# Optimization experiments

Measured on AMD Instinct MI355X. Metric: run time of the kernel, lower is better.

## Reference

```python
import jax, jax.numpy as jnp
import numpy as np

B, D, N, K, V = 32, 256, 2048, 512, 6
COMMIT = 1.0

def setup_inputs() -> dict:
    key = jax.random.key(0)
    k1, k2 = jax.random.split(key)
    inputs = jax.random.normal(k1, (B, D, N), dtype=jnp.float32)
    embeddings = jax.random.normal(k2, (V, D, K), dtype=jnp.float32)
    return {"inputs": inputs, "embeddings": embeddings}

def _vq_layer(residual, emb):
    # residual: (B, D, N); emb: (D, K) codebook
    flat = residual.transpose(0, 2, 1).reshape(-1, D)                # (B*N, D)
    dist = (jnp.sum(flat * flat, axis=1, keepdims=True)
            + jnp.sum(emb * emb, axis=0, keepdims=True)
            - 2.0 * (flat @ emb))                                    # (B*N, K)
    idx = jnp.argmin(dist, axis=1)                                   # (B*N,)
    q = jnp.take(emb.T, idx, axis=0)                                 # (B*N, D) gather
    q = q.reshape(B, N, D).transpose(0, 2, 1)                        # (B, D, N)
    # straight-through estimator
    q_st = residual + jax.lax.stop_gradient(q - residual)
    loss = COMMIT * jnp.mean(jnp.square(jax.lax.stop_gradient(q) - residual))
    return q_st, idx.reshape(B, N), loss

def reference(inputs, embeddings):
    residual = inputs
    q_sum = jnp.zeros_like(inputs)
    tokens = []
    total_loss = jnp.float32(0.0)
    for v in range(V):  # fixed small layer stack
        q, idx, loss = _vq_layer(residual, embeddings[v])
        q_sum = q_sum + q
        tokens.append(idx)
        total_loss = total_loss + loss
        residual = residual - q
    return q_sum, jnp.stack(tokens, axis=0), total_loss
```

## Files before the change

### kernel.cpp

```cpp
#include <hip/hip_runtime.h>

#define B_  32
#define D_  256
#define N_  2048
#define K_  512
#define V_  6
#define DN_ (D_*N_)
#define DK_ (D_*K_)
#define QSZ (B_*D_*N_)
#define TOKSZ (B_*N_)
#define TOK_OFF QSZ
#define LOSS_OFF (QSZ + V_*TOKSZ)
#define MARGIN 0.02f
#define FCAP 16384
#define NBLK (TOKSZ/64)

typedef __attribute__((ext_vector_type(8))) short short8b;
typedef __attribute__((ext_vector_type(4))) float f32x4;

__device__ __forceinline__ unsigned short f2bf(float x) {
  unsigned u = __float_as_uint(x);
  unsigned r = (u + 0x7fffu + ((u >> 16) & 1u)) >> 16;
  return (unsigned short)r;
}
__device__ __forceinline__ float bf2f(unsigned short h) {
  return __uint_as_float(((unsigned)h) << 16);
}
__device__ __forceinline__ unsigned orderf(float f) {
  unsigned u = __float_as_uint(f);
  return (u >> 31) ? ~u : (u | 0x80000000u);
}
__device__ __forceinline__ float unorderf(unsigned u) {
  return __uint_as_float((u & 0x80000000u) ? (u & 0x7fffffffu) : ~u);
}
__device__ __forceinline__ unsigned long long shfl_xor_u64(unsigned long long v, int m) {
  int lo = __shfl_xor((int)(unsigned)(v & 0xffffffffull), m, 64);
  int hi = __shfl_xor((int)(unsigned)(v >> 32), m, 64);
  return ((unsigned long long)(unsigned)hi << 32) | (unsigned)lo;
}

__global__ __launch_bounds__(256) void pack_kernel(const float* __restrict__ emb,
                                                   float* __restrict__ Ef32,
                                                   unsigned short* __restrict__ Ehi,
                                                   unsigned short* __restrict__ Elo) {
  __shared__ float T[64][68];
  const int tid = threadIdx.x;
  const int k0 = blockIdx.x * 64, d0 = blockIdx.y * 64, v = blockIdx.z;
  const float* src = emb + (size_t)v * DK_;
  const int r = tid >> 4, c4 = (tid & 15) * 4;
  #pragma unroll
  for (int i = 0; i < 4; ++i) {
    int d = d0 + r + i * 16;
    float4 x = *(const float4*)(src + (size_t)d * K_ + k0 + c4);
    *(float4*)&T[r + i * 16][c4] = x;
  }
  __syncthreads();
  #pragma unroll
  for (int i = 0; i < 4; ++i) {
    int k = k0 + r + i * 16;
    float4 wv;
    wv.x = T[c4 + 0][r + i * 16];
    wv.y = T[c4 + 1][r + i * 16];
    wv.z = T[c4 + 2][r + i * 16];
    wv.w = T[c4 + 3][r + i * 16];
    size_t o = ((size_t)v * K_ + k) * 256 + d0 + c4;
    *(float4*)(Ef32 + o) = wv;
    ushort4 hv, lv;
    hv.x = f2bf(wv.x); lv.x = f2bf(wv.x - bf2f(hv.x));
    hv.y = f2bf(wv.y); lv.y = f2bf(wv.y - bf2f(hv.y));
    hv.z = f2bf(wv.z); lv.z = f2bf(wv.z - bf2f(hv.z));
    hv.w = f2bf(wv.w); lv.w = f2bf(wv.w - bf2f(hv.w));
    *(ushort4*)(Ehi + o) = hv;
    *(ushort4*)(Elo + o) = lv;
  }
}

__global__ __launch_bounds__(256) void en2_kernel(const float* __restrict__ Ef32,
                                                  float* __restrict__ en2f,
                                                  double* __restrict__ en2d) {
  __shared__ double P[64][4];
  const int tid = threadIdx.x;
  const int k = blockIdx.x * 64 + (tid >> 2), q = tid & 3;
  const float* e = Ef32 + (size_t)k * 256 + q * 64;
  double s = 0.0;
  #pragma unroll 8
  for (int i = 0; i < 64; ++i) { double x = (double)e[i]; s = fma(x, x, s); }
  P[tid >> 2][q] = s;
  __syncthreads();
  if (tid < 64) {
    int k2 = blockIdx.x * 64 + tid;
    double t = (P[tid][0] + P[tid][1]) + (P[tid][2] + P[tid][3]);
    en2d[k2] = t;
    en2f[k2] = (float)t;
  }
}

__global__ __launch_bounds__(256) void transpose_in(const float* __restrict__ in,
                                                    float* __restrict__ Rt) {
  __shared__ float T[64][68];
  const int tid = threadIdx.x;
  const int n0 = blockIdx.x * 64, d0 = blockIdx.y * 64, b = blockIdx.z;
  const float* src = in + (size_t)b * DN_;
  const int r = tid >> 4, c4 = (tid & 15) * 4;
  #pragma unroll
  for (int i = 0; i < 4; ++i) {
    int d = d0 + r + i * 16;
    float4 v = *(const float4*)(src + (size_t)d * N_ + n0 + c4);
    *(float4*)&T[r + i * 16][c4] = v;
  }
  __syncthreads();
  #pragma unroll
  for (int i = 0; i < 4; ++i) {
    int n = n0 + r + i * 16;
    float4 w;
    w.x = T[c4 + 0][r + i * 16];
    w.y = T[c4 + 1][r + i * 16];
    w.z = T[c4 + 2][r + i * 16];
    w.w = T[c4 + 3][r + i * 16];
    *(float4*)(Rt + ((size_t)b * N_ + n) * 256 + d0 + c4) = w;
  }
}

template <bool LAST>
__global__ __launch_bounds__(256, 2) void vq_mfma(
    float* __restrict__ Rt,
    const unsigned short* __restrict__ Ehi, const unsigned short* __restrict__ Elo,
    const float* __restrict__ Ef32v, const float* __restrict__ en2f,
    float* __restrict__ tokOut, float* __restrict__ lossPart,
    int* __restrict__ flagCnt, int* __restrict__ flagList)
{
  __shared__ unsigned short Ahi[8 * 2048];
  __shared__ unsigned short Alo[8 * 2048];
  __shared__ unsigned long long wmin[4][64];
  __shared__ float wsec[4][64];
  __shared__ int sIdx[64];
  __shared__ float wred[4];

  const int tid = threadIdx.x;
  const int lane = tid & 63, w = tid >> 6;
  const int l15 = lane & 15, lg = lane >> 4;
  const int gt0 = blockIdx.x * 64;
  float* rtBase = Rt + (size_t)gt0 * 256;
  const int kb = w * 128;

  const unsigned short* ehiL = Ehi + (size_t)(kb + l15) * 256 + lg * 8;
  const unsigned short* eloL = Elo + (size_t)(kb + l15) * 256 + lg * 8;

  const int stok = tid >> 2, sg = tid & 3;
  #pragma unroll
  for (int c = 0; c < 8; ++c) {
    float4 v0 = *(const float4*)(rtBase + (size_t)stok * 256 + c * 32 + sg * 8);
    float4 v1 = *(const float4*)(rtBase + (size_t)stok * 256 + c * 32 + sg * 8 + 4);
    float xs[8] = {v0.x, v0.y, v0.z, v0.w, v1.x, v1.y, v1.z, v1.w};
    short8b hv, lv;
    #pragma unroll
    for (int j = 0; j < 8; ++j) {
      unsigned short h = f2bf(xs[j]);
      hv[j] = (short)h;
      lv[j] = (short)f2bf(xs[j] - bf2f(h));
    }
    *(short8b*)&Ahi[c * 2048 + sg * 512 + stok * 8] = hv;
    *(short8b*)&Alo[c * 2048 + sg * 512 + stok * 8] = lv;
  }
  __syncthreads();

  f32x4 acc[4][8];
  #pragma unroll
  for (int tt = 0; tt < 4; ++tt)
    #pragma unroll
    for (int kt = 0; kt < 8; ++kt) acc[tt][kt] = (f32x4){0.f, 0.f, 0.f, 0.f};

  float en8[8];
  #pragma unroll
  for (int kt = 0; kt < 8; ++kt) en8[kt] = en2f[kb + kt * 16 + l15];

  #pragma unroll
  for (int c = 0; c < 8; ++c) {
    short8b ah[4], al[4];
    #pragma unroll
    for (int tt = 0; tt < 4; ++tt) {
      ah[tt] = *(const short8b*)&Ahi[c * 2048 + lg * 512 + (tt * 16 + l15) * 8];
      al[tt] = *(const short8b*)&Alo[c * 2048 + lg * 512 + (tt * 16 + l15) * 8];
    }
    #pragma unroll
    for (int kt = 0; kt < 8; ++kt) {
      short8b bh = *(const short8b*)(ehiL + (size_t)kt * 4096 + c * 32);
      short8b bl = *(const short8b*)(eloL + (size_t)kt * 4096 + c * 32);
      #pragma unroll
      for (int tt = 0; tt < 4; ++tt) {
        acc[tt][kt] = __builtin_amdgcn_mfma_f32_16x16x32_bf16(ah[tt], bh, acc[tt][kt], 0, 0, 0);
        acc[tt][kt] = __builtin_amdgcn_mfma_f32_16x16x32_bf16(ah[tt], bl, acc[tt][kt], 0, 0, 0);
        acc[tt][kt] = __builtin_amdgcn_mfma_f32_16x16x32_bf16(al[tt], bh, acc[tt][kt], 0, 0, 0);
      }
    }
  }

  #pragma unroll
  for (int tt = 0; tt < 4; ++tt)
    #pragma unroll
    for (int r = 0; r < 4; ++r) {
      const int token = tt * 16 + lg * 4 + r;
      float dv0 = en8[0] - 2.f * acc[tt][0][r];
      unsigned long long p = ((unsigned long long)orderf(dv0) << 32) | (unsigned)(kb + l15);
      float s = 3.402823466e+38f;
      #pragma unroll
      for (int kt = 1; kt < 8; ++kt) {
        float dv = en8[kt] - 2.f * acc[tt][kt][r];
        unsigned long long pk = ((unsigned long long)orderf(dv) << 32) |
                                (unsigned)(kb + kt * 16 + l15);
        if (pk < p) { s = fminf(s, unorderf((unsigned)(p >> 32))); p = pk; }
        else s = fminf(s, dv);
      }
      #pragma unroll
      for (int m = 1; m <= 8; m <<= 1) {
        unsigned long long po = shfl_xor_u64(p, m);
        float so = __shfl_xor(s, m, 64);
        unsigned long long pmax = (po < p) ? p : po;
        s = fminf(fminf(s, so), unorderf((unsigned)(pmax >> 32)));
        p = (po < p) ? po : p;
      }
      if (l15 == 0) { wmin[w][token] = p; wsec[w][token] = s; }
    }
  __syncthreads();
  if (tid < 64) {
    unsigned long long p = wmin[0][tid]; float s = wsec[0][tid];
    #pragma unroll
    for (int w2 = 1; w2 < 4; ++w2) {
      unsigned long long po = wmin[w2][tid]; float so = wsec[w2][tid];
      unsigned long long pmax = (po < p) ? p : po;
      s = fminf(fminf(s, so), unorderf((unsigned)(pmax >> 32)));
      p = (po < p) ? po : p;
    }
    int kwin = (int)(p & 0xffffffffull);
    sIdx[tid] = kwin;
    tokOut[gt0 + tid] = (float)kwin;
    float bd = unorderf((unsigned)(p >> 32));
    if (s - bd < MARGIN) {
      int pos = atomicAdd(flagCnt, 1);
      if (pos < FCAP) flagList[pos] = gt0 + tid;
    }
  }
  __syncthreads();

  const int uj = tid >> 2, q = tid & 3;
  const int kw = sIdx[uj];
  const float* er = Ef32v + (size_t)kw * 256 + q * 64;
  float* rr = rtBase + (size_t)uj * 256 + q * 64;
  float lacc = 0.f;
  #pragma unroll
  for (int i = 0; i < 8; ++i) {
    const int c = q * 2 + (i >> 2), g = i & 3;
    short8b h8 = *(const short8b*)&Ahi[c * 2048 + g * 512 + uj * 8];
    short8b l8 = *(const short8b*)&Alo[c * 2048 + g * 512 + uj * 8];
    float4 e0 = *(const float4*)(er + i * 8);
    float4 e1 = *(const float4*)(er + i * 8 + 4);
    float rn[8];
    rn[0] = bf2f((unsigned short)h8[0]) + bf2f((unsigned short)l8[0]) - e0.x;
    rn[1] = bf2f((unsigned short)h8[1]) + bf2f((unsigned short)l8[1]) - e0.y;
    rn[2] = bf2f((unsigned short)h8[2]) + bf2f((unsigned short)l8[2]) - e0.z;
    rn[3] = bf2f((unsigned short)h8[3]) + bf2f((unsigned short)l8[3]) - e0.w;
    rn[4] = bf2f((unsigned short)h8[4]) + bf2f((unsigned short)l8[4]) - e1.x;
    rn[5] = bf2f((unsigned short)h8[5]) + bf2f((unsigned short)l8[5]) - e1.y;
    rn[6] = bf2f((unsigned short)h8[6]) + bf2f((unsigned short)l8[6]) - e1.z;
    rn[7] = bf2f((unsigned short)h8[7]) + bf2f((unsigned short)l8[7]) - e1.w;
    if (!LAST) {
      *(float4*)(rr + i * 8)     = make_float4(rn[0], rn[1], rn[2], rn[3]);
      *(float4*)(rr + i * 8 + 4) = make_float4(rn[4], rn[5], rn[6], rn[7]);
    }
    #pragma unroll
    for (int j = 0; j < 8; ++j) lacc += rn[j] * rn[j];
  }
  #pragma unroll
  for (int m = 32; m >= 1; m >>= 1) lacc += __shfl_xor(lacc, m, 64);
  if (lane == 0) wred[w] = lacc;
  __syncthreads();
  if (tid == 0) lossPart[blockIdx.x] = (wred[0] + wred[1]) + (wred[2] + wred[3]);
}

__global__ __launch_bounds__(256) void fixup_kernel(
    const float* __restrict__ inputs, const float* __restrict__ Ef32,
    const double* __restrict__ en2d, float* __restrict__ Rt,
    float* __restrict__ tokens, const int* __restrict__ flagList,
    const int* __restrict__ flagCnt, int v)
{
  __shared__ double rD[256];
  __shared__ double sbd[256];
  __shared__ int sbk[256];
  __shared__ int snk;
  const int tid = threadIdx.x;
  int cnt = flagCnt[0]; if (cnt > FCAP) cnt = FCAP;
  const float* Ev = Ef32 + (size_t)v * DK_;
  for (int i = blockIdx.x; i < cnt; i += gridDim.x) {
    const int gt = flagList[i];
    const int b = gt >> 11, n = gt & (N_ - 1);
    double r = (double)inputs[(size_t)b * DN_ + (size_t)tid * N_ + n];
    for (int u = 0; u < v; ++u) {
      int tu = (int)tokens[u * TOKSZ + gt];
      r -= (double)Ef32[(size_t)u * DK_ + (size_t)tu * 256 + tid];
    }
    rD[tid] = r;
    __syncthreads();
    double best = 1.0e300; int bk = 0;
    #pragma unroll
    for (int half = 0; half < 2; ++half) {
      const int k = tid + half * 256;
      const float* e0 = Ev + (size_t)k * 256;
      double s0 = 0.0, s1 = 0.0, s2 = 0.0, s3 = 0.0;
      #pragma unroll 8
      for (int dd = 0; dd < 256; dd += 4) {
        s0 = fma(rD[dd + 0], (double)e0[dd + 0], s0);
        s1 = fma(rD[dd + 1], (double)e0[dd + 1], s1);
        s2 = fma(rD[dd + 2], (double)e0[dd + 2], s2);
        s3 = fma(rD[dd + 3], (double)e0[dd + 3], s3);
      }
      double dist = en2d[v * K_ + k] - 2.0 * ((s0 + s1) + (s2 + s3));
      if (dist < best) { best = dist; bk = k; }
    }
    sbd[tid] = best; sbk[tid] = bk;
    __syncthreads();
    for (int st = 128; st >= 1; st >>= 1) {
      if (tid < st) {
        double od = sbd[tid + st]; int ok = sbk[tid + st];
        if (od < sbd[tid] || (od == sbd[tid] && ok < sbk[tid])) {
          sbd[tid] = od; sbk[tid] = ok;
        }
      }
      __syncthreads();
    }
    if (tid == 0) {
      int nk = sbk[0];
      int old = (int)tokens[v * TOKSZ + gt];
      if (nk != old) { tokens[v * TOKSZ + gt] = (float)nk; snk = nk; }
      else snk = -1;
    }
    __syncthreads();
    if (snk >= 0)
      Rt[(size_t)gt * 256 + tid] = (float)(rD[tid] - (double)Ev[(size_t)snk * 256 + tid]);
    __syncthreads();
  }
}

__global__ __launch_bounds__(256) void finalize_q(const float* __restrict__ toks,
                                                  const float* __restrict__ Ef32,
                                                  float* __restrict__ out) {
  const int tid = threadIdx.x;
  const int gt = blockIdx.x * 64 + (tid >> 2);
  const int q = tid & 3;
  const int b = gt >> 11, n = gt & (N_ - 1);
  float4 a[16];
  int k0 = (int)toks[gt];
  const float* e0 = Ef32 + (size_t)k0 * 256 + q * 64;
  #pragma unroll
  for (int i = 0; i < 16; ++i) a[i] = ((const float4*)e0)[i];
  #pragma unroll
  for (int v = 1; v < V_; ++v) {
    int kv = (int)toks[v * TOKSZ + gt];
    const float* ev = Ef32 + (size_t)v * DK_ + (size_t)kv * 256 + q * 64;
    #pragma unroll
    for (int i = 0; i < 16; ++i) {
      float4 e = ((const float4*)ev)[i];
      a[i].x += e.x; a[i].y += e.y; a[i].z += e.z; a[i].w += e.w;
    }
  }
  float* dst = out + (size_t)b * DN_ + n;
  #pragma unroll
  for (int i = 0; i < 16; ++i) {
    int d = q * 64 + i * 4;
    dst[(size_t)(d + 0) * N_] = a[i].x;
    dst[(size_t)(d + 1) * N_] = a[i].y;
    dst[(size_t)(d + 2) * N_] = a[i].z;
    dst[(size_t)(d + 3) * N_] = a[i].w;
  }
}

__global__ __launch_bounds__(256) void loss_kernel(const float* __restrict__ part,
                                                   float* __restrict__ out) {
  __shared__ float s[256];
  const int tid = threadIdx.x;
  float a = 0.f;
  for (int i = tid; i < V_ * NBLK; i += 256) a += part[i];
  s[tid] = a;
  __syncthreads();
  for (int st = 128; st >= 1; st >>= 1) {
    if (tid < st) s[tid] += s[tid + st];
    __syncthreads();
  }
  if (tid == 0) out[LOSS_OFF] = s[0] * (1.0f / (float)QSZ);
}

extern "C" void kernel_launch(void* const* d_in, const int* in_sizes, int n_in,
                              void* d_out, int out_size, void* d_ws, size_t ws_size,
                              hipStream_t stream) {
  (void)in_sizes; (void)n_in; (void)out_size; (void)ws_size;
  const float* inputs = (const float*)d_in[0];
  const float* emb    = (const float*)d_in[1];
  float* out = (float*)d_out;
  char* ws = (char*)d_ws;

  unsigned short* Ehi = (unsigned short*)(ws + 0);
  unsigned short* Elo = (unsigned short*)(ws + 1572864);
  float*  Ef32 = (float*)(ws + 3145728);
  float*  en2f = (float*)(ws + 6291456);
  double* en2d = (double*)(ws + 6303744);
  float*  part = (float*)(ws + 6328320);
  int*    flagCnt  = (int*)(ws + 6352896);
  int*    flagList = (int*)(ws + 6352920);

  float* Rt   = out;
  float* toks = out + TOK_OFF;

  hipMemsetAsync(flagCnt, 0, V_ * sizeof(int), stream);
  pack_kernel<<<dim3(8, 4, 6), 256, 0, stream>>>(emb, Ef32, Ehi, Elo);
  en2_kernel<<<48, 256, 0, stream>>>(Ef32, en2f, en2d);
  transpose_in<<<dim3(32, 4, 32), 256, 0, stream>>>(inputs, Rt);

  for (int v = 0; v < V_; ++v) {
    const unsigned short* ehi = Ehi + (size_t)v * DK_;
    const unsigned short* elo = Elo + (size_t)v * DK_;
    const float* ef = Ef32 + (size_t)v * DK_;
    if (v < V_ - 1)
      vq_mfma<false><<<NBLK, 256, 0, stream>>>(Rt, ehi, elo, ef, en2f + v * K_,
                                               toks + v * TOKSZ, part + v * NBLK,
                                               flagCnt + v, flagList + v * FCAP);
    else
      vq_mfma<true><<<NBLK, 256, 0, stream>>>(Rt, ehi, elo, ef, en2f + v * K_,
                                              toks + v * TOKSZ, part + v * NBLK,
                                              flagCnt + v, flagList + v * FCAP);
    fixup_kernel<<<512, 256, 0, stream>>>(inputs, Ef32, en2d, Rt, toks,
                                          flagList + v * FCAP, flagCnt + v, v);
  }
  finalize_q<<<NBLK, 256, 0, stream>>>(toks, Ef32, out);
  loss_kernel<<<1, 256, 0, stream>>>(part, out);
}
```

Baseline: 879.6 us.

## Store residual as split bf16 hi/lo in global memory and halve tokens per block

The residual is now kept in global memory as pre-split bf16 hi/lo arrays instead of fp32. The MFMA kernel reads A fragments directly from global memory, so the per-block LDS staging and the conversion pass go away. Tokens per block drop from 64 to 32 and the occupancy hint rises to 4 blocks per CU, which gives more blocks and fewer accumulators per thread but less reuse of the codebook B loads per block. The residual update re-splits into hi/lo on write, and the fixup kernel writes the same format. The partial-loss buffer grows, so the flag offsets in the workspace move.

```diff
diff --git a/kernel.cpp b/kernel.cpp
--- a/kernel.cpp
+++ b/kernel.cpp
@@ -13,7 +13,8 @@
 #define LOSS_OFF (QSZ + V_*TOKSZ)
 #define MARGIN 0.02f
 #define FCAP 16384
-#define NBLK (TOKSZ/64)
+#define TPB_ 32
+#define NBLK (TOKSZ/TPB_)
 
 typedef __attribute__((ext_vector_type(8))) short short8b;
 typedef __attribute__((ext_vector_type(4))) float f32x4;
@@ -95,8 +96,9 @@
   }
 }
 
-__global__ __launch_bounds__(256) void transpose_in(const float* __restrict__ in,
-                                                    float* __restrict__ Rt) {
+__global__ __launch_bounds__(256) void split_in(const float* __restrict__ in,
+                                                unsigned short* __restrict__ Rhi,
+                                                unsigned short* __restrict__ Rlo) {
   __shared__ float T[64][68];
   const int tid = threadIdx.x;
   const int n0 = blockIdx.x * 64, d0 = blockIdx.y * 64, b = blockIdx.z;
@@ -117,86 +119,72 @@
     w.y = T[c4 + 1][r + i * 16];
     w.z = T[c4 + 2][r + i * 16];
     w.w = T[c4 + 3][r + i * 16];
-    *(float4*)(Rt + ((size_t)b * N_ + n) * 256 + d0 + c4) = w;
+    ushort4 hv, lv;
+    hv.x = f2bf(w.x); lv.x = f2bf(w.x - bf2f(hv.x));
+    hv.y = f2bf(w.y); lv.y = f2bf(w.y - bf2f(hv.y));
+    hv.z = f2bf(w.z); lv.z = f2bf(w.z - bf2f(hv.z));
+    hv.w = f2bf(w.w); lv.w = f2bf(w.w - bf2f(hv.w));
+    size_t o = ((size_t)b * N_ + n) * 256 + d0 + c4;
+    *(ushort4*)(Rhi + o) = hv;
+    *(ushort4*)(Rlo + o) = lv;
   }
 }
 
 template <bool LAST>
-__global__ __launch_bounds__(256, 2) void vq_mfma(
-    float* __restrict__ Rt,
+__global__ __launch_bounds__(256, 4) void vq_mfma(
+    unsigned short* __restrict__ Rhi, unsigned short* __restrict__ Rlo,
     const unsigned short* __restrict__ Ehi, const unsigned short* __restrict__ Elo,
     const float* __restrict__ Ef32v, const float* __restrict__ en2f,
     float* __restrict__ tokOut, float* __restrict__ lossPart,
     int* __restrict__ flagCnt, int* __restrict__ flagList)
 {
-  __shared__ unsigned short Ahi[8 * 2048];
-  __shared__ unsigned short Alo[8 * 2048];
-  __shared__ unsigned long long wmin[4][64];
-  __shared__ float wsec[4][64];
-  __shared__ int sIdx[64];
+  __shared__ unsigned long long wmin[4][TPB_];
+  __shared__ float wsec[4][TPB_];
+  __shared__ int sIdx[TPB_];
   __shared__ float wred[4];
 
   const int tid = threadIdx.x;
   const int lane = tid & 63, w = tid >> 6;
   const int l15 = lane & 15, lg = lane >> 4;
-  const int gt0 = blockIdx.x * 64;
-  float* rtBase = Rt + (size_t)gt0 * 256;
+  const int gt0 = blockIdx.x * TPB_;
   const int kb = w * 128;
 
   const unsigned short* ehiL = Ehi + (size_t)(kb + l15) * 256 + lg * 8;
   const unsigned short* eloL = Elo + (size_t)(kb + l15) * 256 + lg * 8;
-
-  const int stok = tid >> 2, sg = tid & 3;
+  const unsigned short* ahiL = Rhi + (size_t)(gt0 + l15) * 256 + lg * 8;
+  const unsigned short* aloL = Rlo + (size_t)(gt0 + l15) * 256 + lg * 8;
+
+  f32x4 acc[2][8];
+  #pragma unroll
+  for (int tt = 0; tt < 2; ++tt)
+    #pragma unroll
+    for (int kt = 0; kt < 8; ++kt) acc[tt][kt] = (f32x4){0.f, 0.f, 0.f, 0.f};
+
   #pragma unroll
   for (int c = 0; c < 8; ++c) {
-    float4 v0 = *(const float4*)(rtBase + (size_t)stok * 256 + c * 32 + sg * 8);
-    float4 v1 = *(const float4*)(rtBase + (size_t)stok * 256 + c * 32 + sg * 8 + 4);
-    float xs[8] = {v0.x, v0.y, v0.z, v0.w, v1.x, v1.y, v1.z, v1.w};
-    short8b hv, lv;
-    #pragma unroll
-    for (int j = 0; j < 8; ++j) {
-      unsigned short h = f2bf(xs[j]);
-      hv[j] = (short)h;
-      lv[j] = (short)f2bf(xs[j] - bf2f(h));
-    }
-    *(short8b*)&Ahi[c * 2048 + sg * 512 + stok * 8] = hv;
-    *(short8b*)&Alo[c * 2048 + sg * 512 + stok * 8] = lv;
-  }
-  __syncthreads();
-
-  f32x4 acc[4][8];
-  #pragma unroll
-  for (int tt = 0; tt < 4; ++tt)
-    #pragma unroll
-    for (int kt = 0; kt < 8; ++kt) acc[tt][kt] = (f32x4){0.f, 0.f, 0.f, 0.f};
-
-  float en8[8];
-  #pragma unroll
-  for (int kt = 0; kt < 8; ++kt) en8[kt] = en2f[kb + kt * 16 + l15];
-
-  #pragma unroll
-  for (int c = 0; c < 8; ++c) {
-    short8b ah[4], al[4];
-    #pragma unroll
-    for (int tt = 0; tt < 4; ++tt) {
-      ah[tt] = *(const short8b*)&Ahi[c * 2048 + lg * 512 + (tt * 16 + l15) * 8];
-      al[tt] = *(const short8b*)&Alo[c * 2048 + lg * 512 + (tt * 16 + l15) * 8];
-    }
+    short8b ah0 = *(const short8b*)(ahiL + c * 32);
+    short8b ah1 = *(const short8b*)(ahiL + 4096 + c * 32);
+    short8b al0 = *(const short8b*)(aloL + c * 32);
+    short8b al1 = *(const short8b*)(aloL + 4096 + c * 32);
     #pragma unroll
     for (int kt = 0; kt < 8; ++kt) {
       short8b bh = *(const short8b*)(ehiL + (size_t)kt * 4096 + c * 32);
       short8b bl = *(const short8b*)(eloL + (size_t)kt * 4096 + c * 32);
-      #pragma unroll
-      for (int tt = 0; tt < 4; ++tt) {
-        acc[tt][kt] = __builtin_amdgcn_mfma_f32_16x16x32_bf16(ah[tt], bh, acc[tt][kt], 0, 0, 0);
-        acc[tt][kt] = __builtin_amdgcn_mfma_f32_16x16x32_bf16(ah[tt], bl, acc[tt][kt], 0, 0, 0);
-        acc[tt][kt] = __builtin_amdgcn_mfma_f32_16x16x32_bf16(al[tt], bh, acc[tt][kt], 0, 0, 0);
-      }
-    }
-  }
-
-  #pragma unroll
-  for (int tt = 0; tt < 4; ++tt)
+      acc[0][kt] = __builtin_amdgcn_mfma_f32_16x16x32_bf16(ah0, bh, acc[0][kt], 0, 0, 0);
+      acc[0][kt] = __builtin_amdgcn_mfma_f32_16x16x32_bf16(ah0, bl, acc[0][kt], 0, 0, 0);
+      acc[0][kt] = __builtin_amdgcn_mfma_f32_16x16x32_bf16(al0, bh, acc[0][kt], 0, 0, 0);
+      acc[1][kt] = __builtin_amdgcn_mfma_f32_16x16x32_bf16(ah1, bh, acc[1][kt], 0, 0, 0);
+      acc[1][kt] = __builtin_amdgcn_mfma_f32_16x16x32_bf16(ah1, bl, acc[1][kt], 0, 0, 0);
+      acc[1][kt] = __builtin_amdgcn_mfma_f32_16x16x32_bf16(al1, bh, acc[1][kt], 0, 0, 0);
+    }
+  }
+
+  float en8[8];
+  #pragma unroll
+  for (int kt = 0; kt < 8; ++kt) en8[kt] = en2f[kb + kt * 16 + l15];
+
+  #pragma unroll
+  for (int tt = 0; tt < 2; ++tt)
     #pragma unroll
     for (int r = 0; r < 4; ++r) {
       const int token = tt * 16 + lg * 4 + r;
@@ -222,7 +210,7 @@
       if (l15 == 0) { wmin[w][token] = p; wsec[w][token] = s; }
     }
   __syncthreads();
-  if (tid < 64) {
+  if (tid < TPB_) {
     unsigned long long p = wmin[0][tid]; float s = wsec[0][tid];
     #pragma unroll
     for (int w2 = 1; w2 < 4; ++w2) {
@@ -242,33 +230,33 @@
   }
   __syncthreads();
 
-  const int uj = tid >> 2, q = tid & 3;
+  const int uj = tid >> 3, q = tid & 7;
   const int kw = sIdx[uj];
-  const float* er = Ef32v + (size_t)kw * 256 + q * 64;
-  float* rr = rtBase + (size_t)uj * 256 + q * 64;
+  const unsigned short* rh = Rhi + (size_t)(gt0 + uj) * 256 + q * 32;
+  const unsigned short* rl = Rlo + (size_t)(gt0 + uj) * 256 + q * 32;
+  const float* er = Ef32v + (size_t)kw * 256 + q * 32;
   float lacc = 0.f;
   #pragma unroll
-  for (int i = 0; i < 8; ++i) {
-    const int c = q * 2 + (i >> 2), g = i & 3;
-    short8b h8 = *(const short8b*)&Ahi[c * 2048 + g * 512 + uj * 8];
-    short8b l8 = *(const short8b*)&Alo[c * 2048 + g * 512 + uj * 8];
+  for (int i = 0; i < 4; ++i) {
+    short8b h8 = *(const short8b*)(rh + i * 8);
+    short8b l8 = *(const short8b*)(rl + i * 8);
     float4 e0 = *(const float4*)(er + i * 8);
     float4 e1 = *(const float4*)(er + i * 8 + 4);
-    float rn[8];
-    rn[0] = bf2f((unsigned short)h8[0]) + bf2f((unsigned short)l8[0]) - e0.x;
-    rn[1] = bf2f((unsigned short)h8[1]) + bf2f((unsigned short)l8[1]) - e0.y;
-    rn[2] = bf2f((unsigned short)h8[2]) + bf2f((unsigned short)l8[2]) - e0.z;
-    rn[3] = bf2f((unsigned short)h8[3]) + bf2f((unsigned short)l8[3]) - e0.w;
-    rn[4] = bf2f((unsigned short)h8[4]) + bf2f((unsigned short)l8[4]) - e1.x;
-    rn[5] = bf2f((unsigned short)h8[5]) + bf2f((unsigned short)l8[5]) - e1.y;
-    rn[6] = bf2f((unsigned short)h8[6]) + bf2f((unsigned short)l8[6]) - e1.z;
-    rn[7] = bf2f((unsigned short)h8[7]) + bf2f((unsigned short)l8[7]) - e1.w;
+    float ee[8] = {e0.x, e0.y, e0.z, e0.w, e1.x, e1.y, e1.z, e1.w};
+    short8b nh, nl;
+    #pragma unroll
+    for (int j = 0; j < 8; ++j) {
+      float rv = bf2f((unsigned short)h8[j]) + bf2f((unsigned short)l8[j]);
+      float rn = rv - ee[j];
+      unsigned short hh = f2bf(rn);
+      nh[j] = (short)hh;
+      nl[j] = (short)f2bf(rn - bf2f(hh));
+      lacc += rn * rn;
+    }
     if (!LAST) {
-      *(float4*)(rr + i * 8)     = make_float4(rn[0], rn[1], rn[2], rn[3]);
-      *(float4*)(rr + i * 8 + 4) = make_float4(rn[4], rn[5], rn[6], rn[7]);
-    }
-    #pragma unroll
-    for (int j = 0; j < 8; ++j) lacc += rn[j] * rn[j];
+      *(short8b*)(const_cast<unsigned short*>(rh) + i * 8) = nh;
+      *(short8b*)(const_cast<unsigned short*>(rl) + i * 8) = nl;
+    }
   }
   #pragma unroll
   for (int m = 32; m >= 1; m >>= 1) lacc += __shfl_xor(lacc, m, 64);
@@ -279,7 +267,8 @@
 
 __global__ __launch_bounds__(256) void fixup_kernel(
     const float* __restrict__ inputs, const float* __restrict__ Ef32,
-    const double* __restrict__ en2d, float* __restrict__ Rt,
+    const double* __restrict__ en2d,
+    unsigned short* __restrict__ Rhi, unsigned short* __restrict__ Rlo,
     float* __restrict__ tokens, const int* __restrict__ flagList,
     const int* __restrict__ flagCnt, int v)
 {
@@ -334,8 +323,12 @@
       else snk = -1;
     }
     __syncthreads();
-    if (snk >= 0)
-      Rt[(size_t)gt * 256 + tid] = (float)(rD[tid] - (double)Ev[(size_t)snk * 256 + tid]);
+    if (snk >= 0) {
+      float x = (float)(rD[tid] - (double)Ev[(size_t)snk * 256 + tid]);
+      unsigned short hh = f2bf(x);
+      Rhi[(size_t)gt * 256 + tid] = hh;
+      Rlo[(size_t)gt * 256 + tid] = f2bf(x - bf2f(hh));
+    }
     __syncthreads();
   }
 }
@@ -403,32 +396,33 @@
   float*  en2f = (float*)(ws + 6291456);
   double* en2d = (double*)(ws + 6303744);
   float*  part = (float*)(ws + 6328320);
-  int*    flagCnt  = (int*)(ws + 6352896);
-  int*    flagList = (int*)(ws + 6352920);
-
-  float* Rt   = out;
+  int*    flagCnt  = (int*)(ws + 6377472);
+  int*    flagList = (int*)(ws + 6377496);
+
+  unsigned short* Rhi = (unsigned short*)out;
+  unsigned short* Rlo = Rhi + (size_t)TOKSZ * 256;
   float* toks = out + TOK_OFF;
 
   hipMemsetAsync(flagCnt, 0, V_ * sizeof(int), stream);
   pack_kernel<<<dim3(8, 4, 6), 256, 0, stream>>>(emb, Ef32, Ehi, Elo);
   en2_kernel<<<48, 256, 0, stream>>>(Ef32, en2f, en2d);
-  transpose_in<<<dim3(32, 4, 32), 256, 0, stream>>>(inputs, Rt);
+  split_in<<<dim3(32, 4, 32), 256, 0, stream>>>(inputs, Rhi, Rlo);
 
   for (int v = 0; v < V_; ++v) {
     const unsigned short* ehi = Ehi + (size_t)v * DK_;
     const unsigned short* elo = Elo + (size_t)v * DK_;
     const float* ef = Ef32 + (size_t)v * DK_;
     if (v < V_ - 1)
-      vq_mfma<false><<<NBLK, 256, 0, stream>>>(Rt, ehi, elo, ef, en2f + v * K_,
+      vq_mfma<false><<<NBLK, 256, 0, stream>>>(Rhi, Rlo, ehi, elo, ef, en2f + v * K_,
                                                toks + v * TOKSZ, part + v * NBLK,
                                                flagCnt + v, flagList + v * FCAP);
     else
-      vq_mfma<true><<<NBLK, 256, 0, stream>>>(Rt, ehi, elo, ef, en2f + v * K_,
+      vq_mfma<true><<<NBLK, 256, 0, stream>>>(Rhi, Rlo, ehi, elo, ef, en2f + v * K_,
                                               toks + v * TOKSZ, part + v * NBLK,
                                               flagCnt + v, flagList + v * FCAP);
-    fixup_kernel<<<512, 256, 0, stream>>>(inputs, Ef32, en2d, Rt, toks,
+    fixup_kernel<<<512, 256, 0, stream>>>(inputs, Ef32, en2d, Rhi, Rlo, toks,
                                           flagList + v * FCAP, flagCnt + v, v);
   }
-  finalize_q<<<NBLK, 256, 0, stream>>>(toks, Ef32, out);
+  finalize_q<<<TOKSZ / 64, 256, 0, stream>>>(toks, Ef32, out);
   loss_kernel<<<1, 256, 0, stream>>>(part, out);
 }
```

Result: slower. 1.538 ms (+74.9%).

## Fuse all RVQ layers and fp64 fixup into one persistent-per-tile kernel

Applied to the files above, without the earlier changes.

Replaces the separate transpose, six per-layer VQ kernels and six fixup kernels with one kernel. Each 64-token block keeps its residual resident in LDS as bf16 hi/lo pairs across all layers, and it reads the inputs transposed directly from global memory. Near-tie tokens are refined in place in fp64 using a ballot mask, which removes the global atomic flag list and the fixup launches. The residual no longer goes through global memory between layers, which cuts traffic and launch overhead. In exchange, fixup work now serialises inside each block, the input load is strided and uncoalesced per element, and the residual is re-rounded to bf16 hi/lo each layer, which could shift precision.

```diff
diff --git a/kernel.cpp b/kernel.cpp
--- a/kernel.cpp
+++ b/kernel.cpp
@@ -12,8 +12,8 @@
 #define TOK_OFF QSZ
 #define LOSS_OFF (QSZ + V_*TOKSZ)
 #define MARGIN 0.02f
-#define FCAP 16384
-#define NBLK (TOKSZ/64)
+#define TPB 64
+#define NBLK (TOKSZ/TPB)
 
 typedef __attribute__((ext_vector_type(8))) short short8b;
 typedef __attribute__((ext_vector_type(4))) float f32x4;
@@ -95,247 +95,214 @@
   }
 }
 
-__global__ __launch_bounds__(256) void transpose_in(const float* __restrict__ in,
-                                                    float* __restrict__ Rt) {
-  __shared__ float T[64][68];
-  const int tid = threadIdx.x;
-  const int n0 = blockIdx.x * 64, d0 = blockIdx.y * 64, b = blockIdx.z;
-  const float* src = in + (size_t)b * DN_;
-  const int r = tid >> 4, c4 = (tid & 15) * 4;
-  #pragma unroll
-  for (int i = 0; i < 4; ++i) {
-    int d = d0 + r + i * 16;
-    float4 v = *(const float4*)(src + (size_t)d * N_ + n0 + c4);
-    *(float4*)&T[r + i * 16][c4] = v;
-  }
-  __syncthreads();
-  #pragma unroll
-  for (int i = 0; i < 4; ++i) {
-    int n = n0 + r + i * 16;
-    float4 w;
-    w.x = T[c4 + 0][r + i * 16];
-    w.y = T[c4 + 1][r + i * 16];
-    w.z = T[c4 + 2][r + i * 16];
-    w.w = T[c4 + 3][r + i * 16];
-    *(float4*)(Rt + ((size_t)b * N_ + n) * 256 + d0 + c4) = w;
-  }
-}
-
-template <bool LAST>
-__global__ __launch_bounds__(256, 2) void vq_mfma(
-    float* __restrict__ Rt,
+__global__ __launch_bounds__(256, 2) void rvq_fused(
+    const float* __restrict__ inputs,
     const unsigned short* __restrict__ Ehi, const unsigned short* __restrict__ Elo,
-    const float* __restrict__ Ef32v, const float* __restrict__ en2f,
-    float* __restrict__ tokOut, float* __restrict__ lossPart,
-    int* __restrict__ flagCnt, int* __restrict__ flagList)
+    const float* __restrict__ Ef32, const float* __restrict__ en2f,
+    const double* __restrict__ en2d,
+    float* __restrict__ tokens, float* __restrict__ lossPart)
 {
   __shared__ unsigned short Ahi[8 * 2048];
   __shared__ unsigned short Alo[8 * 2048];
-  __shared__ unsigned long long wmin[4][64];
-  __shared__ float wsec[4][64];
-  __shared__ int sIdx[64];
+  __shared__ unsigned long long wmin[4][TPB];
+  __shared__ float wsec[4][TPB];
+  __shared__ int sIdx[TPB];
+  __shared__ int sHist[V_][TPB];
+  __shared__ double rD[256];
+  __shared__ double sbd[256];
+  __shared__ int sbk[256];
+  __shared__ unsigned long long sFlag;
   __shared__ float wred[4];
 
   const int tid = threadIdx.x;
   const int lane = tid & 63, w = tid >> 6;
   const int l15 = lane & 15, lg = lane >> 4;
-  const int gt0 = blockIdx.x * 64;
-  float* rtBase = Rt + (size_t)gt0 * 256;
+  const int gt0 = blockIdx.x * TPB;
+  const int b = gt0 >> 11, n0 = gt0 & (N_ - 1);
   const int kb = w * 128;
 
-  const unsigned short* ehiL = Ehi + (size_t)(kb + l15) * 256 + lg * 8;
-  const unsigned short* eloL = Elo + (size_t)(kb + l15) * 256 + lg * 8;
-
-  const int stok = tid >> 2, sg = tid & 3;
-  #pragma unroll
-  for (int c = 0; c < 8; ++c) {
-    float4 v0 = *(const float4*)(rtBase + (size_t)stok * 256 + c * 32 + sg * 8);
-    float4 v1 = *(const float4*)(rtBase + (size_t)stok * 256 + c * 32 + sg * 8 + 4);
-    float xs[8] = {v0.x, v0.y, v0.z, v0.w, v1.x, v1.y, v1.z, v1.w};
-    short8b hv, lv;
-    #pragma unroll
-    for (int j = 0; j < 8; ++j) {
-      unsigned short h = f2bf(xs[j]);
-      hv[j] = (short)h;
-      lv[j] = (short)f2bf(xs[j] - bf2f(h));
-    }
-    *(short8b*)&Ahi[c * 2048 + sg * 512 + stok * 8] = hv;
-    *(short8b*)&Alo[c * 2048 + sg * 512 + stok * 8] = lv;
+  {
+    const float* src = inputs + (size_t)b * DN_ + n0 + lane;
+    #pragma unroll
+    for (int cc = 0; cc < 2; ++cc) {
+      const int c = w * 2 + cc;
+      #pragma unroll
+      for (int g = 0; g < 4; ++g) {
+        short8b hv, lv;
+        #pragma unroll
+        for (int e = 0; e < 8; ++e) {
+          float x = src[(size_t)(c * 32 + g * 8 + e) * N_];
+          unsigned short h = f2bf(x);
+          hv[e] = (short)h;
+          lv[e] = (short)f2bf(x - bf2f(h));
+        }
+        *(short8b*)&Ahi[c * 2048 + g * 512 + lane * 8] = hv;
+        *(short8b*)&Alo[c * 2048 + g * 512 + lane * 8] = lv;
+      }
+    }
   }
   __syncthreads();
 
-  f32x4 acc[4][8];
-  #pragma unroll
-  for (int tt = 0; tt < 4; ++tt)
-    #pragma unroll
-    for (int kt = 0; kt < 8; ++kt) acc[tt][kt] = (f32x4){0.f, 0.f, 0.f, 0.f};
-
-  float en8[8];
-  #pragma unroll
-  for (int kt = 0; kt < 8; ++kt) en8[kt] = en2f[kb + kt * 16 + l15];
-
-  #pragma unroll
-  for (int c = 0; c < 8; ++c) {
-    short8b ah[4], al[4];
-    #pragma unroll
-    for (int tt = 0; tt < 4; ++tt) {
-      ah[tt] = *(const short8b*)&Ahi[c * 2048 + lg * 512 + (tt * 16 + l15) * 8];
-      al[tt] = *(const short8b*)&Alo[c * 2048 + lg * 512 + (tt * 16 + l15) * 8];
-    }
-    #pragma unroll
-    for (int kt = 0; kt < 8; ++kt) {
-      short8b bh = *(const short8b*)(ehiL + (size_t)kt * 4096 + c * 32);
-      short8b bl = *(const short8b*)(eloL + (size_t)kt * 4096 + c * 32);
+  for (int v = 0; v < V_; ++v) {
+    const unsigned short* ehiL = Ehi + (size_t)v * DK_ + (size_t)(kb + l15) * 256 + lg * 8;
+    const unsigned short* eloL = Elo + (size_t)v * DK_ + (size_t)(kb + l15) * 256 + lg * 8;
+    const float* Ef32v = Ef32 + (size_t)v * DK_;
+
+    f32x4 acc[4][8];
+    #pragma unroll
+    for (int tt = 0; tt < 4; ++tt)
+      #pragma unroll
+      for (int kt = 0; kt < 8; ++kt) acc[tt][kt] = (f32x4){0.f, 0.f, 0.f, 0.f};
+
+    #pragma unroll
+    for (int c = 0; c < 8; ++c) {
+      short8b ah[4], al[4];
       #pragma unroll
       for (int tt = 0; tt < 4; ++tt) {
-        acc[tt][kt] = __builtin_amdgcn_mfma_f32_16x16x32_bf16(ah[tt], bh, acc[tt][kt], 0, 0, 0);
-        acc[tt][kt] = __builtin_amdgcn_mfma_f32_16x16x32_bf16(ah[tt], bl, acc[tt][kt], 0, 0, 0);
-        acc[tt][kt] = __builtin_amdgcn_mfma_f32_16x16x32_bf16(al[tt], bh, acc[tt][kt], 0, 0, 0);
-      }
-    }
-  }
-
-  #pragma unroll
-  for (int tt = 0; tt < 4; ++tt)
-    #pragma unroll
-    for (int r = 0; r < 4; ++r) {
-      const int token = tt * 16 + lg * 4 + r;
-      float dv0 = en8[0] - 2.f * acc[tt][0][r];
-      unsigned long long p = ((unsigned long long)orderf(dv0) << 32) | (unsigned)(kb + l15);
-      float s = 3.402823466e+38f;
-      #pragma unroll
-      for (int kt = 1; kt < 8; ++kt) {
-        float dv = en8[kt] - 2.f * acc[tt][kt][r];
-        unsigned long long pk = ((unsigned long long)orderf(dv) << 32) |
-                                (unsigned)(kb + kt * 16 + l15);
-        if (pk < p) { s = fminf(s, unorderf((unsigned)(p >> 32))); p = pk; }
-        else s = fminf(s, dv);
-      }
-      #pragma unroll
-      for (int m = 1; m <= 8; m <<= 1) {
-        unsigned long long po = shfl_xor_u64(p, m);
-        float so = __shfl_xor(s, m, 64);
+        ah[tt] = *(const short8b*)&Ahi[c * 2048 + lg * 512 + (tt * 16 + l15) * 8];
+        al[tt] = *(const short8b*)&Alo[c * 2048 + lg * 512 + (tt * 16 + l15) * 8];
+      }
+      #pragma unroll
+      for (int kt = 0; kt < 8; ++kt) {
+        short8b bh = *(const short8b*)(ehiL + (size_t)kt * 4096 + c * 32);
+        short8b bl = *(const short8b*)(eloL + (size_t)kt * 4096 + c * 32);
+        #pragma unroll
+        for (int tt = 0; tt < 4; ++tt) {
+          acc[tt][kt] = __builtin_amdgcn_mfma_f32_16x16x32_bf16(ah[tt], bh, acc[tt][kt], 0, 0, 0);
+          acc[tt][kt] = __builtin_amdgcn_mfma_f32_16x16x32_bf16(ah[tt], bl, acc[tt][kt], 0, 0, 0);
+          acc[tt][kt] = __builtin_amdgcn_mfma_f32_16x16x32_bf16(al[tt], bh, acc[tt][kt], 0, 0, 0);
+        }
+      }
+    }
+
+    float en8[8];
+    #pragma unroll
+    for (int kt = 0; kt < 8; ++kt) en8[kt] = en2f[v * K_ + kb + kt * 16 + l15];
+
+    #pragma unroll
+    for (int tt = 0; tt < 4; ++tt)
+      #pragma unroll
+      for (int r = 0; r < 4; ++r) {
+        const int token = tt * 16 + lg * 4 + r;
+        float dv0 = en8[0] - 2.f * acc[tt][0][r];
+        unsigned long long p = ((unsigned long long)orderf(dv0) << 32) | (unsigned)(kb + l15);
+        float s = 3.402823466e+38f;
+        #pragma unroll
+        for (int kt = 1; kt < 8; ++kt) {
+          float dv = en8[kt] - 2.f * acc[tt][kt][r];
+          unsigned long long pk = ((unsigned long long)orderf(dv) << 32) |
+                                  (unsigned)(kb + kt * 16 + l15);
+          if (pk < p) { s = fminf(s, unorderf((unsigned)(p >> 32))); p = pk; }
+          else s = fminf(s, dv);
+        }
+        #pragma unroll
+        for (int m = 1; m <= 8; m <<= 1) {
+          unsigned long long po = shfl_xor_u64(p, m);
+          float so = __shfl_xor(s, m, 64);
+          unsigned long long pmax = (po < p) ? p : po;
+          s = fminf(fminf(s, so), unorderf((unsigned)(pmax >> 32)));
+          p = (po < p) ? po : p;
+        }
+        if (l15 == 0) { wmin[w][token] = p; wsec[w][token] = s; }
+      }
+    __syncthreads();
+    if (tid < TPB) {
+      unsigned long long p = wmin[0][tid]; float s = wsec[0][tid];
+      #pragma unroll
+      for (int w2 = 1; w2 < 4; ++w2) {
+        unsigned long long po = wmin[w2][tid]; float so = wsec[w2][tid];
         unsigned long long pmax = (po < p) ? p : po;
         s = fminf(fminf(s, so), unorderf((unsigned)(pmax >> 32)));
         p = (po < p) ? po : p;
       }
-      if (l15 == 0) { wmin[w][token] = p; wsec[w][token] = s; }
-    }
-  __syncthreads();
-  if (tid < 64) {
-    unsigned long long p = wmin[0][tid]; float s = wsec[0][tid];
-    #pragma unroll
-    for (int w2 = 1; w2 < 4; ++w2) {
-      unsigned long long po = wmin[w2][tid]; float so = wsec[w2][tid];
-      unsigned long long pmax = (po < p) ? p : po;
-      s = fminf(fminf(s, so), unorderf((unsigned)(pmax >> 32)));
-      p = (po < p) ? po : p;
-    }
-    int kwin = (int)(p & 0xffffffffull);
-    sIdx[tid] = kwin;
-    tokOut[gt0 + tid] = (float)kwin;
-    float bd = unorderf((unsigned)(p >> 32));
-    if (s - bd < MARGIN) {
-      int pos = atomicAdd(flagCnt, 1);
-      if (pos < FCAP) flagList[pos] = gt0 + tid;
-    }
-  }
-  __syncthreads();
-
-  const int uj = tid >> 2, q = tid & 3;
-  const int kw = sIdx[uj];
-  const float* er = Ef32v + (size_t)kw * 256 + q * 64;
-  float* rr = rtBase + (size_t)uj * 256 + q * 64;
-  float lacc = 0.f;
-  #pragma unroll
-  for (int i = 0; i < 8; ++i) {
-    const int c = q * 2 + (i >> 2), g = i & 3;
-    short8b h8 = *(const short8b*)&Ahi[c * 2048 + g * 512 + uj * 8];
-    short8b l8 = *(const short8b*)&Alo[c * 2048 + g * 512 + uj * 8];
-    float4 e0 = *(const float4*)(er + i * 8);
-    float4 e1 = *(const float4*)(er + i * 8 + 4);
-    float rn[8];
-    rn[0] = bf2f((unsigned short)h8[0]) + bf2f((unsigned short)l8[0]) - e0.x;
-    rn[1] = bf2f((unsigned short)h8[1]) + bf2f((unsigned short)l8[1]) - e0.y;
-    rn[2] = bf2f((unsigned short)h8[2]) + bf2f((unsigned short)l8[2]) - e0.z;
-    rn[3] = bf2f((unsigned short)h8[3]) + bf2f((unsigned short)l8[3]) - e0.w;
-    rn[4] = bf2f((unsigned short)h8[4]) + bf2f((unsigned short)l8[4]) - e1.x;
-    rn[5] = bf2f((unsigned short)h8[5]) + bf2f((unsigned short)l8[5]) - e1.y;
-    rn[6] = bf2f((unsigned short)h8[6]) + bf2f((unsigned short)l8[6]) - e1.z;
-    rn[7] = bf2f((unsigned short)h8[7]) + bf2f((unsigned short)l8[7]) - e1.w;
-    if (!LAST) {
-      *(float4*)(rr + i * 8)     = make_float4(rn[0], rn[1], rn[2], rn[3]);
-      *(float4*)(rr + i * 8 + 4) = make_float4(rn[4], rn[5], rn[6], rn[7]);
-    }
-    #pragma unroll
-    for (int j = 0; j < 8; ++j) lacc += rn[j] * rn[j];
-  }
-  #pragma unroll
-  for (int m = 32; m >= 1; m >>= 1) lacc += __shfl_xor(lacc, m, 64);
-  if (lane == 0) wred[w] = lacc;
-  __syncthreads();
-  if (tid == 0) lossPart[blockIdx.x] = (wred[0] + wred[1]) + (wred[2] + wred[3]);
-}
-
-__global__ __launch_bounds__(256) void fixup_kernel(
-    const float* __restrict__ inputs, const float* __restrict__ Ef32,
-    const double* __restrict__ en2d, float* __restrict__ Rt,
-    float* __restrict__ tokens, const int* __restrict__ flagList,
-    const int* __restrict__ flagCnt, int v)
-{
-  __shared__ double rD[256];
-  __shared__ double sbd[256];
-  __shared__ int sbk[256];
-  __shared__ int snk;
-  const int tid = threadIdx.x;
-  int cnt = flagCnt[0]; if (cnt > FCAP) cnt = FCAP;
-  const float* Ev = Ef32 + (size_t)v * DK_;
-  for (int i = blockIdx.x; i < cnt; i += gridDim.x) {
-    const int gt = flagList[i];
-    const int b = gt >> 11, n = gt & (N_ - 1);
-    double r = (double)inputs[(size_t)b * DN_ + (size_t)tid * N_ + n];
-    for (int u = 0; u < v; ++u) {
-      int tu = (int)tokens[u * TOKSZ + gt];
-      r -= (double)Ef32[(size_t)u * DK_ + (size_t)tu * 256 + tid];
-    }
-    rD[tid] = r;
-    __syncthreads();
-    double best = 1.0e300; int bk = 0;
-    #pragma unroll
-    for (int half = 0; half < 2; ++half) {
-      const int k = tid + half * 256;
-      const float* e0 = Ev + (size_t)k * 256;
-      double s0 = 0.0, s1 = 0.0, s2 = 0.0, s3 = 0.0;
-      #pragma unroll 8
-      for (int dd = 0; dd < 256; dd += 4) {
-        s0 = fma(rD[dd + 0], (double)e0[dd + 0], s0);
-        s1 = fma(rD[dd + 1], (double)e0[dd + 1], s1);
-        s2 = fma(rD[dd + 2], (double)e0[dd + 2], s2);
-        s3 = fma(rD[dd + 3], (double)e0[dd + 3], s3);
-      }
-      double dist = en2d[v * K_ + k] - 2.0 * ((s0 + s1) + (s2 + s3));
-      if (dist < best) { best = dist; bk = k; }
-    }
-    sbd[tid] = best; sbk[tid] = bk;
-    __syncthreads();
-    for (int st = 128; st >= 1; st >>= 1) {
-      if (tid < st) {
-        double od = sbd[tid + st]; int ok = sbk[tid + st];
-        if (od < sbd[tid] || (od == sbd[tid] && ok < sbk[tid])) {
-          sbd[tid] = od; sbk[tid] = ok;
-        }
-      }
+      sIdx[tid] = (int)(p & 0xffffffffull);
+      float bd = unorderf((unsigned)(p >> 32));
+      unsigned long long fl = __ballot(s - bd < MARGIN);
+      if (tid == 0) sFlag = fl;
+    }
+    __syncthreads();
+
+    unsigned long long mask = sFlag;
+    while (mask) {
+      const int j = __builtin_ctzll(mask);
+      mask &= mask - 1;
+      double r = (double)inputs[(size_t)b * DN_ + (size_t)tid * N_ + (n0 + j)];
+      for (int u = 0; u < v; ++u)
+        r -= (double)Ef32[(size_t)u * DK_ + (size_t)sHist[u][j] * 256 + tid];
+      rD[tid] = r;
       __syncthreads();
-    }
-    if (tid == 0) {
-      int nk = sbk[0];
-      int old = (int)tokens[v * TOKSZ + gt];
-      if (nk != old) { tokens[v * TOKSZ + gt] = (float)nk; snk = nk; }
-      else snk = -1;
-    }
-    __syncthreads();
-    if (snk >= 0)
-      Rt[(size_t)gt * 256 + tid] = (float)(rD[tid] - (double)Ev[(size_t)snk * 256 + tid]);
+      double best = 1.0e300; int bk = 0;
+      #pragma unroll
+      for (int half = 0; half < 2; ++half) {
+        const int k = tid + half * 256;
+        const float* e0 = Ef32v + (size_t)k * 256;
+        double s0 = 0.0, s1 = 0.0, s2 = 0.0, s3 = 0.0;
+        #pragma unroll 8
+        for (int dd = 0; dd < 256; dd += 4) {
+          s0 = fma(rD[dd + 0], (double)e0[dd + 0], s0);
+          s1 = fma(rD[dd + 1], (double)e0[dd + 1], s1);
+          s2 = fma(rD[dd + 2], (double)e0[dd + 2], s2);
+          s3 = fma(rD[dd + 3], (double)e0[dd + 3], s3);
+        }
+        double dist = en2d[v * K_ + k] - 2.0 * ((s0 + s1) + (s2 + s3));
+        if (dist < best) { best = dist; bk = k; }
+      }
+      sbd[tid] = best; sbk[tid] = bk;
+      __syncthreads();
+      for (int st = 128; st >= 1; st >>= 1) {
+        if (tid < st) {
+          double od = sbd[tid + st]; int ok = sbk[tid + st];
+          if (od < sbd[tid] || (od == sbd[tid] && ok < sbk[tid])) {
+            sbd[tid] = od; sbk[tid] = ok;
+          }
+        }
+        __syncthreads();
+      }
+      if (tid == 0) sIdx[j] = sbk[0];
+      __syncthreads();
+    }
+
+    if (tid < TPB) {
+      sHist[v][tid] = sIdx[tid];
+      tokens[(size_t)v * TOKSZ + gt0 + tid] = (float)sIdx[tid];
+    }
+    __syncthreads();
+
+    const int uj = tid >> 2, q = tid & 3;
+    const int kw = sIdx[uj];
+    const float* er = Ef32v + (size_t)kw * 256 + q * 64;
+    float lacc = 0.f;
+    #pragma unroll
+    for (int i = 0; i < 8; ++i) {
+      const int c = q * 2 + (i >> 2), g = i & 3;
+      unsigned short* ph = &Ahi[c * 2048 + g * 512 + uj * 8];
+      unsigned short* pl = &Alo[c * 2048 + g * 512 + uj * 8];
+      short8b h8 = *(const short8b*)ph;
+      short8b l8 = *(const short8b*)pl;
+      float4 e0 = *(const float4*)(er + i * 8);
+      float4 e1 = *(const float4*)(er + i * 8 + 4);
+      float ee[8] = {e0.x, e0.y, e0.z, e0.w, e1.x, e1.y, e1.z, e1.w};
+      short8b nh, nl;
+      #pragma unroll
+      for (int jj = 0; jj < 8; ++jj) {
+        float rv = bf2f((unsigned short)h8[jj]) + bf2f((unsigned short)l8[jj]);
+        float rn = rv - ee[jj];
+        unsigned short hh = f2bf(rn);
+        nh[jj] = (short)hh;
+        nl[jj] = (short)f2bf(rn - bf2f(hh));
+        lacc += rn * rn;
+      }
+      if (v < V_ - 1) {
+        *(short8b*)ph = nh;
+        *(short8b*)pl = nl;
+      }
+    }
+    #pragma unroll
+    for (int m = 32; m >= 1; m >>= 1) lacc += __shfl_xor(lacc, m, 64);
+    if (lane == 0) wred[w] = lacc;
+    __syncthreads();
+    if (tid == 0)
+      lossPart[(size_t)v * NBLK + blockIdx.x] = (wred[0] + wred[1]) + (wred[2] + wred[3]);
     __syncthreads();
   }
 }
@@ -403,32 +370,12 @@
   float*  en2f = (float*)(ws + 6291456);
   double* en2d = (double*)(ws + 6303744);
   float*  part = (float*)(ws + 6328320);
-  int*    flagCnt  = (int*)(ws + 6352896);
-  int*    flagList = (int*)(ws + 6352920);
-
-  float* Rt   = out;
+
   float* toks = out + TOK_OFF;
 
-  hipMemsetAsync(flagCnt, 0, V_ * sizeof(int), stream);
   pack_kernel<<<dim3(8, 4, 6), 256, 0, stream>>>(emb, Ef32, Ehi, Elo);
   en2_kernel<<<48, 256, 0, stream>>>(Ef32, en2f, en2d);
-  transpose_in<<<dim3(32, 4, 32), 256, 0, stream>>>(inputs, Rt);
-
-  for (int v = 0; v < V_; ++v) {
-    const unsigned short* ehi = Ehi + (size_t)v * DK_;
-    const unsigned short* elo = Elo + (size_t)v * DK_;
-    const float* ef = Ef32 + (size_t)v * DK_;
-    if (v < V_ - 1)
-      vq_mfma<false><<<NBLK, 256, 0, stream>>>(Rt, ehi, elo, ef, en2f + v * K_,
-                                               toks + v * TOKSZ, part + v * NBLK,
-                                               flagCnt + v, flagList + v * FCAP);
-    else
-      vq_mfma<true><<<NBLK, 256, 0, stream>>>(Rt, ehi, elo, ef, en2f + v * K_,
-                                              toks + v * TOKSZ, part + v * NBLK,
-                                              flagCnt + v, flagList + v * FCAP);
-    fixup_kernel<<<512, 256, 0, stream>>>(inputs, Ef32, en2d, Rt, toks,
-                                          flagList + v * FCAP, flagCnt + v, v);
-  }
-  finalize_q<<<NBLK, 256, 0, stream>>>(toks, Ef32, out);
+  rvq_fused<<<NBLK, 256, 0, stream>>>(inputs, Ehi, Elo, Ef32, en2f, en2d, toks, part);
+  finalize_q<<<TOKSZ / 64, 256, 0, stream>>>(toks, Ef32, out);
   loss_kernel<<<1, 256, 0, stream>>>(part, out);
 }
```

Measured after the change: 730.4 us. 1.2x faster.
